# Kernel tuning notes

Hardware: AMD Instinct MI355X
Metric: run time of the kernel (lower is better)

## Reference

```python
import jax, jax.numpy as jnp
import numpy as np

N_NODES = 100000
N_EDGES = 600000
N_GRAPHS = 64
BN_EPS = 1e-5


def setup_inputs() -> dict:
    key = jax.random.key(0)
    ks = jax.random.split(key, 32)
    inp = {
        "x": jax.random.normal(ks[0], (N_NODES, 128), dtype=jnp.float32),
        "edge_index": jax.random.randint(ks[1], (2, N_EDGES), 0, N_NODES, dtype=jnp.int64),
        "batch": jnp.sort(jax.random.randint(ks[2], (N_NODES,), 0, N_GRAPHS, dtype=jnp.int64)),
    }
    dims = [(128, 64, 64), (64, 64, 64), (64, 64, 96)]  # (in, hid, out) per GIN layer
    ki = 3
    for i, (d_in, d_hid, d_out) in enumerate(dims):
        inp[f"l{i}_w1"] = jax.random.normal(ks[ki], (d_in, d_hid), dtype=jnp.float32) * 0.05; ki += 1
        inp[f"l{i}_b1"] = jnp.zeros((d_hid,), dtype=jnp.float32)
        inp[f"l{i}_w2"] = jax.random.normal(ks[ki], (d_hid, d_out), dtype=jnp.float32) * 0.05; ki += 1
        inp[f"l{i}_b2"] = jnp.zeros((d_out,), dtype=jnp.float32)
        inp[f"bn{i}_g"] = jax.random.uniform(ks[ki], (d_out,), minval=0.5, maxval=1.5, dtype=jnp.float32); ki += 1
        inp[f"bn{i}_b"] = jax.random.normal(ks[ki], (d_out,), dtype=jnp.float32) * 0.05; ki += 1
        inp[f"bn{i}_m"] = jax.random.normal(ks[ki], (d_out,), dtype=jnp.float32) * 0.05; ki += 1
        inp[f"bn{i}_v"] = jax.random.uniform(ks[ki], (d_out,), minval=0.5, maxval=1.5, dtype=jnp.float32); ki += 1
    return inp


def _gin_layer(x, src, dst, w1, b1, w2, b2, g, bb, m, v):
    # GINConv (eps=0): h_i = MLP(x_i + sum_{j: j->i} x_j)
    aggr = jax.ops.segment_sum(x[src], dst, num_segments=N_NODES)
    h = x + aggr
    h = jax.nn.relu(h @ w1 + b1) @ w2 + b2
    # eval-mode BatchNorm1d + ReLU
    h = (h - m) * jax.lax.rsqrt(v + BN_EPS) * g + bb
    return jax.nn.relu(h)


def reference(x, edge_index, batch,
              l0_w1, l0_b1, l0_w2, l0_b2, bn0_g, bn0_b, bn0_m, bn0_v,
              l1_w1, l1_b1, l1_w2, l1_b2, bn1_g, bn1_b, bn1_m, bn1_v,
              l2_w1, l2_b1, l2_w2, l2_b2, bn2_g, bn2_b, bn2_m, bn2_v):
    src, dst = edge_index[0], edge_index[1]
    h = _gin_layer(x, src, dst, l0_w1, l0_b1, l0_w2, l0_b2, bn0_g, bn0_b, bn0_m, bn0_v)
    h = _gin_layer(h, src, dst, l1_w1, l1_b1, l1_w2, l1_b2, bn1_g, bn1_b, bn1_m, bn1_v)
    h = _gin_layer(h, src, dst, l2_w1, l2_b1, l2_w2, l2_b2, bn2_g, bn2_b, bn2_m, bn2_v)
    # global mean pool over graphs
    sums = jax.ops.segment_sum(h, batch, num_segments=N_GRAPHS)
    counts = jax.ops.segment_sum(jnp.ones((h.shape[0],), dtype=h.dtype), batch, num_segments=N_GRAPHS)
    return sums / jnp.maximum(counts, 1.0)[:, None]
```

## Files before the change

### kernel.cpp

```cpp
#include <hip/hip_runtime.h>

#define N_NODES 100000
#define N_GRAPHS 64
#define N_EDGES 600000
#define BN_EPS 1e-5f

__global__ void deg_hist_kernel(const int* __restrict__ dst,
                                int* __restrict__ deg, int n_edges) {
    int e = blockIdx.x * blockDim.x + threadIdx.x;
    if (e < n_edges) atomicAdd(&deg[dst[e]], 1);
}

__global__ void scan1_kernel(const int* __restrict__ deg, int* __restrict__ excl,
                             int* __restrict__ partials, int n) {
    __shared__ int s[1024];
    int i = blockIdx.x * 1024 + threadIdx.x;
    int v = (i < n) ? deg[i] : 0;
    s[threadIdx.x] = v;
    __syncthreads();
    for (int off = 1; off < 1024; off <<= 1) {
        int t = (threadIdx.x >= (unsigned)off) ? s[threadIdx.x - off] : 0;
        __syncthreads();
        s[threadIdx.x] += t;
        __syncthreads();
    }
    if (i < n) excl[i] = s[threadIdx.x] - v;
    if (threadIdx.x == 1023) partials[blockIdx.x] = s[1023];
}

__global__ void scan2_kernel(int* partials, int nb) {
    __shared__ int s[128];
    int t = threadIdx.x;
    int v = (t < nb) ? partials[t] : 0;
    s[t] = v;
    __syncthreads();
    for (int off = 1; off < 128; off <<= 1) {
        int u = (t >= off) ? s[t - off] : 0;
        __syncthreads();
        s[t] += u;
        __syncthreads();
    }
    if (t < nb) partials[t] = s[t] - v;
}

__global__ void scan3_kernel(int* __restrict__ rowptr, const int* __restrict__ partials,
                             int n, int total) {
    int i = blockIdx.x * blockDim.x + threadIdx.x;
    if (i < n) rowptr[i] += partials[i >> 10];
    else if (i == n) rowptr[n] = total;
}

__global__ void csr_fill_kernel(const int* __restrict__ src, const int* __restrict__ dst,
                                const int* __restrict__ rowptr, int* __restrict__ cursor,
                                int* __restrict__ eids, int n_edges) {
    int e = blockIdx.x * blockDim.x + threadIdx.x;
    if (e >= n_edges) return;
    int t = dst[e];
    int pos = rowptr[t] + atomicAdd(&cursor[t], 1);
    eids[pos] = src[e];
}

__global__ void graph_bounds_kernel(const int* __restrict__ batch,
                                    int* __restrict__ gstart, int n_nodes) {
    int n = blockIdx.x * blockDim.x + threadIdx.x;
    if (n >= n_nodes) return;
    if (n == 0) {
        for (int g = 0; g <= batch[0]; ++g) gstart[g] = 0;
    } else {
        int b0 = batch[n - 1], b1 = batch[n];
        for (int g = b0 + 1; g <= b1; ++g) gstart[g] = n;
    }
    if (n == n_nodes - 1) {
        for (int g = batch[n] + 1; g <= N_GRAPHS; ++g) gstart[g] = n_nodes;
    }
}

__global__ void prep_kernel(const float* __restrict__ w1, const float* __restrict__ w2,
                            const float* __restrict__ b2, const float* __restrict__ g,
                            const float* __restrict__ bb, const float* __restrict__ m,
                            const float* __restrict__ v,
                            float* __restrict__ w1T, float* __restrict__ w2sT,
                            float* __restrict__ bias2, int DIN, int DOUT) {
    int i = blockIdx.x * blockDim.x + threadIdx.x;
    if (i < 64 * DIN) {
        int j = i / DIN, k = i % DIN;
        w1T[i] = w1[k * 64 + j];
    }
    int i2 = i - 64 * DIN;
    if (i2 >= 0 && i2 < DOUT * 64) {
        int c = i2 / 64, j = i2 % 64;
        float s = g[c] * rsqrtf(v[c] + BN_EPS);
        w2sT[i2] = w2[j * DOUT + c] * s;
    }
    int i3 = i2 - DOUT * 64;
    if (i3 >= 0 && i3 < DOUT) {
        float s = g[i3] * rsqrtf(v[i3] + BN_EPS);
        bias2[i3] = (b2[i3] - m[i3]) * s + bb[i3];
    }
}

__global__ __launch_bounds__(256)
void pre_gemm_kernel(const float* __restrict__ x, const float* __restrict__ w1T,
                     float* __restrict__ y, int n_nodes) {
    __shared__ float w1s[64 * 128];
    const int tid = threadIdx.x;
    const long base = (long)blockIdx.x * 64;

    const float4* gw1 = (const float4*)w1T;
    for (int i4 = tid; i4 < 16 * 128; i4 += 256) {
        int row = i4 >> 5, k4 = i4 & 31;
        *(float4*)&w1s[row * 128 + ((k4 ^ ((row >> 2) & 7)) << 2)] = gw1[i4];
    }
    __syncthreads();

    const int jg = tid & 15, ng = tid >> 4, xw = jg & 7;
    const float* wp = &w1s[(jg * 4) * 128];
    const float4* xv = (const float4*)x;
    long r[4];
    #pragma unroll
    for (int i = 0; i < 4; ++i) {
        long rr = base + ng * 4 + i;
        r[i] = (rr < n_nodes) ? rr : (n_nodes - 1);
    }
    float acc[4][4] = {};
    #pragma unroll 4
    for (int k4 = 0; k4 < 32; ++k4) {
        const int ko = (k4 ^ xw) << 2;
        float4 w0 = *(const float4*)&wp[0 * 128 + ko];
        float4 w1v = *(const float4*)&wp[1 * 128 + ko];
        float4 w2v = *(const float4*)&wp[2 * 128 + ko];
        float4 w3v = *(const float4*)&wp[3 * 128 + ko];
        #pragma unroll
        for (int i = 0; i < 4; ++i) {
            float4 a = xv[r[i] * 32 + k4];
            acc[i][0] = fmaf(a.x, w0.x, fmaf(a.y, w0.y, fmaf(a.z, w0.z, fmaf(a.w, w0.w, acc[i][0]))));
            acc[i][1] = fmaf(a.x, w1v.x, fmaf(a.y, w1v.y, fmaf(a.z, w1v.z, fmaf(a.w, w1v.w, acc[i][1]))));
            acc[i][2] = fmaf(a.x, w2v.x, fmaf(a.y, w2v.y, fmaf(a.z, w2v.z, fmaf(a.w, w2v.w, acc[i][2]))));
            acc[i][3] = fmaf(a.x, w3v.x, fmaf(a.y, w3v.y, fmaf(a.z, w3v.z, fmaf(a.w, w3v.w, acc[i][3]))));
        }
    }
    #pragma unroll
    for (int i = 0; i < 4; ++i) {
        long n = base + ng * 4 + i;
        if (n < n_nodes) {
            float4 v = {acc[i][0], acc[i][1], acc[i][2], acc[i][3]};
            *(float4*)(y + n * 64 + jg * 4) = v;
        }
    }
}

__global__ __launch_bounds__(256)
void gather64_kernel(const float* __restrict__ y, const int* __restrict__ rowptr,
                     const int* __restrict__ eids, const float* __restrict__ b1,
                     float* __restrict__ t, int n_nodes) {
    int node = blockIdx.x * 16 + (threadIdx.x >> 4);
    if (node >= n_nodes) return;
    int f4 = threadIdx.x & 15;
    const float4* yv = (const float4*)y;
    float4 acc = yv[(long)node * 16 + f4];
    int b = rowptr[node], e = rowptr[node + 1];
    int i = b;
    for (; i + 3 < e; i += 4) {
        int s0 = eids[i], s1 = eids[i + 1], s2 = eids[i + 2], s3 = eids[i + 3];
        float4 r0 = yv[(long)s0 * 16 + f4];
        float4 r1 = yv[(long)s1 * 16 + f4];
        float4 r2 = yv[(long)s2 * 16 + f4];
        float4 r3 = yv[(long)s3 * 16 + f4];
        acc.x += (r0.x + r1.x) + (r2.x + r3.x);
        acc.y += (r0.y + r1.y) + (r2.y + r3.y);
        acc.z += (r0.z + r1.z) + (r2.z + r3.z);
        acc.w += (r0.w + r1.w) + (r2.w + r3.w);
    }
    for (; i < e; ++i) {
        int s = eids[i];
        float4 r = yv[(long)s * 16 + f4];
        acc.x += r.x; acc.y += r.y; acc.z += r.z; acc.w += r.w;
    }
    float4 bv = ((const float4*)b1)[f4];
    float4 o;
    o.x = fmaxf(acc.x + bv.x, 0.0f);
    o.y = fmaxf(acc.y + bv.y, 0.0f);
    o.z = fmaxf(acc.z + bv.z, 0.0f);
    o.w = fmaxf(acc.w + bv.w, 0.0f);
    ((float4*)t)[(long)node * 16 + f4] = o;
}

__global__ __launch_bounds__(256)
void fused_mid_kernel(const float* __restrict__ t, const float* __restrict__ w2sT,
                      const float* __restrict__ bias2, const float* __restrict__ w1nT,
                      float* __restrict__ ynext, int n_nodes) {
    constexpr int SS = 68;
    __shared__ float sT[64 * SS];
    __shared__ float wbuf[64 * 64];
    const int tid = threadIdx.x;
    const long base = (long)blockIdx.x * 64;

    const float4* gw2 = (const float4*)w2sT;
    for (int i4 = tid; i4 < 16 * 64; i4 += 256) {
        int row = i4 >> 4, k4 = i4 & 15;
        *(float4*)&wbuf[row * 64 + ((k4 ^ ((row >> 2) & 7)) << 2)] = gw2[i4];
    }
    __syncthreads();

    const int jg = tid & 15, ng = tid >> 4, xw = jg & 7;
    const float4* tv = (const float4*)(t + base * 64);

    float h[4][4];
    {
        const float* wp = &wbuf[(jg * 4) * 64];
        float acc[4][4] = {};
        #pragma unroll 4
        for (int k4 = 0; k4 < 16; ++k4) {
            const int ko = (k4 ^ xw) << 2;
            float4 w0 = *(const float4*)&wp[0 * 64 + ko];
            float4 w1v = *(const float4*)&wp[1 * 64 + ko];
            float4 w2v = *(const float4*)&wp[2 * 64 + ko];
            float4 w3v = *(const float4*)&wp[3 * 64 + ko];
            #pragma unroll
            for (int i = 0; i < 4; ++i) {
                float4 a = tv[(ng * 4 + i) * 16 + k4];
                acc[i][0] = fmaf(a.x, w0.x, fmaf(a.y, w0.y, fmaf(a.z, w0.z, fmaf(a.w, w0.w, acc[i][0]))));
                acc[i][1] = fmaf(a.x, w1v.x, fmaf(a.y, w1v.y, fmaf(a.z, w1v.z, fmaf(a.w, w1v.w, acc[i][1]))));
                acc[i][2] = fmaf(a.x, w2v.x, fmaf(a.y, w2v.y, fmaf(a.z, w2v.z, fmaf(a.w, w2v.w, acc[i][2]))));
                acc[i][3] = fmaf(a.x, w3v.x, fmaf(a.y, w3v.y, fmaf(a.z, w3v.z, fmaf(a.w, w3v.w, acc[i][3]))));
            }
        }
        float4 bv = *(const float4*)&bias2[jg * 4];
        #pragma unroll
        for (int i = 0; i < 4; ++i) {
            h[i][0] = fmaxf(acc[i][0] + bv.x, 0.0f);
            h[i][1] = fmaxf(acc[i][1] + bv.y, 0.0f);
            h[i][2] = fmaxf(acc[i][2] + bv.z, 0.0f);
            h[i][3] = fmaxf(acc[i][3] + bv.w, 0.0f);
        }
    }
    __syncthreads();

    #pragma unroll
    for (int i = 0; i < 4; ++i) {
        float4 hv = {h[i][0], h[i][1], h[i][2], h[i][3]};
        *(float4*)&sT[(ng * 4 + i) * SS + jg * 4] = hv;
    }
    const float4* gw1n = (const float4*)w1nT;
    for (int i4 = tid; i4 < 16 * 64; i4 += 256) {
        int row = i4 >> 4, k4 = i4 & 15;
        *(float4*)&wbuf[row * 64 + ((k4 ^ ((row >> 2) & 7)) << 2)] = gw1n[i4];
    }
    __syncthreads();

    {
        const float* ap = &sT[(ng * 4) * SS];
        const float* wp = &wbuf[(jg * 4) * 64];
        float acc[4][4] = {};
        #pragma unroll 4
        for (int k4 = 0; k4 < 16; ++k4) {
            const int ko = (k4 ^ xw) << 2;
            float4 w0 = *(const float4*)&wp[0 * 64 + ko];
            float4 w1v = *(const float4*)&wp[1 * 64 + ko];
            float4 w2v = *(const float4*)&wp[2 * 64 + ko];
            float4 w3v = *(const float4*)&wp[3 * 64 + ko];
            #pragma unroll
            for (int i = 0; i < 4; ++i) {
                float4 a = *(const float4*)&ap[i * SS + k4 * 4];
                acc[i][0] = fmaf(a.x, w0.x, fmaf(a.y, w0.y, fmaf(a.z, w0.z, fmaf(a.w, w0.w, acc[i][0]))));
                acc[i][1] = fmaf(a.x, w1v.x, fmaf(a.y, w1v.y, fmaf(a.z, w1v.z, fmaf(a.w, w1v.w, acc[i][1]))));
                acc[i][2] = fmaf(a.x, w2v.x, fmaf(a.y, w2v.y, fmaf(a.z, w2v.z, fmaf(a.w, w2v.w, acc[i][2]))));
                acc[i][3] = fmaf(a.x, w3v.x, fmaf(a.y, w3v.y, fmaf(a.z, w3v.z, fmaf(a.w, w3v.w, acc[i][3]))));
            }
        }
        #pragma unroll
        for (int i = 0; i < 4; ++i) {
            long n = base + ng * 4 + i;
            if (n < n_nodes) {
                float4 v = {acc[i][0], acc[i][1], acc[i][2], acc[i][3]};
                *(float4*)(ynext + n * 64 + jg * 4) = v;
            }
        }
    }
}

__global__ __launch_bounds__(256)
void fused_final_kernel(const float* __restrict__ t, const float* __restrict__ w2sT,
                        const float* __restrict__ bias2, float* __restrict__ out,
                        int n_nodes) {
    constexpr int CPT = 6;
    __shared__ float w2s[96 * 64];
    const int tid = threadIdx.x;
    const long base = (long)blockIdx.x * 64;

    const float4* gw2 = (const float4*)w2sT;
    for (int i4 = tid; i4 < 96 * 16; i4 += 256) {
        int row = i4 >> 4, k4 = i4 & 15;
        *(float4*)&w2s[row * 64 + ((k4 ^ ((row / CPT) & 7)) << 2)] = gw2[i4];
    }
    __syncthreads();

    const int cg = tid & 15, ng = tid >> 4, xw = cg & 7;
    const float4* tv = (const float4*)(t + base * 64);
    const float* wp = &w2s[(cg * CPT) * 64];
    float acc[4][CPT] = {};
    #pragma unroll 4
    for (int k4 = 0; k4 < 16; ++k4) {
        const int ko = (k4 ^ xw) << 2;
        float4 wv[CPT];
        #pragma unroll
        for (int c = 0; c < CPT; ++c) wv[c] = *(const float4*)&wp[c * 64 + ko];
        #pragma unroll
        for (int i = 0; i < 4; ++i) {
            float4 h = tv[(ng * 4 + i) * 16 + k4];
            #pragma unroll
            for (int c = 0; c < CPT; ++c)
                acc[i][c] = fmaf(h.x, wv[c].x, fmaf(h.y, wv[c].y, fmaf(h.z, wv[c].z, fmaf(h.w, wv[c].w, acc[i][c]))));
        }
    }
    float bv[CPT];
    #pragma unroll
    for (int c = 0; c < CPT; ++c) bv[c] = bias2[cg * CPT + c];
    #pragma unroll
    for (int i = 0; i < 4; ++i) {
        long n = base + ng * 4 + i;
        if (n < n_nodes) {
            float* op = out + n * 96 + cg * CPT;
            #pragma unroll
            for (int c = 0; c < CPT; ++c) op[c] = fmaxf(acc[i][c] + bv[c], 0.0f);
        }
    }
}

#define POOL_SPLIT 16
__global__ __launch_bounds__(192)
void pool_seg_kernel(const float* __restrict__ h, const int* __restrict__ gstart,
                     float* __restrict__ sums) {
    int g = blockIdx.x >> 4;
    int s = blockIdx.x & 15;
    int lo = gstart[g], hi = gstart[g + 1];
    int len = hi - lo;
    int seg = (len + POOL_SPLIT - 1) / POOL_SPLIT;
    int a = lo + s * seg;
    int b = a + seg; if (b > hi) b = hi;

    int f4 = threadIdx.x % 24;
    int chain = threadIdx.x / 24;
    const float4* hv = (const float4*)h;
    float4 acc = {0.0f, 0.0f, 0.0f, 0.0f};
    for (int n = a + chain; n < b; n += 8) {
        float4 v = hv[(long)n * 24 + f4];
        acc.x += v.x; acc.y += v.y; acc.z += v.z; acc.w += v.w;
    }
    __shared__ float4 red[8][24];
    red[chain][f4] = acc;
    __syncthreads();
    if (threadIdx.x < 24) {
        float4 t = red[0][threadIdx.x];
        #pragma unroll
        for (int c = 1; c < 8; ++c) {
            float4 r = red[c][threadIdx.x];
            t.x += r.x; t.y += r.y; t.z += r.z; t.w += r.w;
        }
        float* sp = &sums[g * 96 + threadIdx.x * 4];
        atomicAdd(sp + 0, t.x);
        atomicAdd(sp + 1, t.y);
        atomicAdd(sp + 2, t.z);
        atomicAdd(sp + 3, t.w);
    }
}

__global__ void finalize_kernel(const float* __restrict__ sums,
                                const int* __restrict__ gstart,
                                float* __restrict__ out) {
    int i = blockIdx.x * blockDim.x + threadIdx.x;
    if (i >= N_GRAPHS * 96) return;
    int g = i / 96;
    float cnt = (float)(gstart[g + 1] - gstart[g]);
    out[i] = sums[i] / fmaxf(cnt, 1.0f);
}

static inline int cdiv_l(long a, int b) { return (int)((a + b - 1) / b); }

extern "C" void kernel_launch(void* const* d_in, const int* in_sizes, int n_in,
                              void* d_out, int out_size, void* d_ws, size_t ws_size,
                              hipStream_t stream) {
    const float* x     = (const float*)d_in[0];
    const int*   ei    = (const int*)d_in[1];
    const int*   src   = ei;
    const int*   dst   = ei + N_EDGES;
    const int*   batch = (const int*)d_in[2];

    const float* P[3][8];
    int p = 3;
    for (int l = 0; l < 3; ++l)
        for (int q = 0; q < 8; ++q)
            P[l][q] = (const float*)d_in[p++];

    const long NP = N_NODES + 64;
    float* ws   = (float*)d_ws;
    float* yT   = ws;
    float* gB   = yT + NP * 64;
    float* h2   = gB + NP * 64;
    float* q    = h2 + NP * 96;
    float* w1T[3], *w2sT[3], *bias2[3];
    for (int l = 0; l < 3; ++l) {
        w1T[l] = q;   q += 64 * 128;
        w2sT[l] = q;  q += 96 * 64;
        bias2[l] = q; q += 96;
    }
    float* sums   = q;
    int* gstart   = (int*)(sums + N_GRAPHS * 96);
    int* deg      = gstart + 72;
    int* cursor   = deg + N_NODES;
    int* partials = cursor + N_NODES;
    int* rowptr   = partials + 128;
    int* eids     = rowptr + (N_NODES + 1);

    const int B = 256;
    const int DIN[3]  = {128, 64, 64};
    const int DOUT[3] = {64, 64, 96};

    for (int l = 0; l < 3; ++l) {
        int tot = 64 * DIN[l] + 64 * DOUT[l] + DOUT[l];
        prep_kernel<<<cdiv_l(tot, B), B, 0, stream>>>(
            P[l][0], P[l][2], P[l][3], P[l][4], P[l][5], P[l][6], P[l][7],
            w1T[l], w2sT[l], bias2[l], DIN[l], DOUT[l]);
    }

    hipMemsetAsync(deg, 0, (size_t)(2 * N_NODES + 128) * sizeof(int), stream);
    deg_hist_kernel<<<cdiv_l(N_EDGES, B), B, 0, stream>>>(dst, deg, N_EDGES);
    int nblk = cdiv_l(N_NODES, 1024);
    scan1_kernel<<<nblk, 1024, 0, stream>>>(deg, rowptr, partials, N_NODES);
    scan2_kernel<<<1, 128, 0, stream>>>(partials, nblk);
    scan3_kernel<<<cdiv_l(N_NODES + 1, B), B, 0, stream>>>(rowptr, partials, N_NODES, N_EDGES);
    csr_fill_kernel<<<cdiv_l(N_EDGES, B), B, 0, stream>>>(src, dst, rowptr, cursor, eids, N_EDGES);
    graph_bounds_kernel<<<cdiv_l(N_NODES, B), B, 0, stream>>>(batch, gstart, N_NODES);

    const int ntiles = cdiv_l(N_NODES, 64);
    const int ngather = cdiv_l(N_NODES, 16);

    pre_gemm_kernel<<<ntiles, 256, 0, stream>>>(x, w1T[0], yT, N_NODES);
    gather64_kernel<<<ngather, 256, 0, stream>>>(yT, rowptr, eids, P[0][1], gB, N_NODES);
    fused_mid_kernel<<<ntiles, 256, 0, stream>>>(
        gB, w2sT[0], bias2[0], w1T[1], yT, N_NODES);
    gather64_kernel<<<ngather, 256, 0, stream>>>(yT, rowptr, eids, P[1][1], gB, N_NODES);
    fused_mid_kernel<<<ntiles, 256, 0, stream>>>(
        gB, w2sT[1], bias2[1], w1T[2], yT, N_NODES);
    gather64_kernel<<<ngather, 256, 0, stream>>>(yT, rowptr, eids, P[2][1], gB, N_NODES);
    fused_final_kernel<<<ntiles, 256, 0, stream>>>(
        gB, w2sT[2], bias2[2], h2, N_NODES);

    hipMemsetAsync(sums, 0, (size_t)(N_GRAPHS * 96) * sizeof(float), stream);
    pool_seg_kernel<<<N_GRAPHS * POOL_SPLIT, 192, 0, stream>>>(h2, gstart, sums);
    finalize_kernel<<<cdiv_l(N_GRAPHS * 96, B), B, 0, stream>>>(
        sums, gstart, (float*)d_out);
}
```

Baseline: 433.4 us.

## Fuse neighbor gather into MLP kernels with 128-node tiles and ping-pong buffers

Each per-layer gather kernel is folded into the following MLP kernel: the block gathers neighbor rows for its 128-node tile straight into shared memory and then runs both GEMMs, so the intermediate buffer no longer makes a global round trip. Tiles and blocks grow to 128 nodes and 512 threads, the three prep launches become one 2D launch, and pooling writes per-split partials that finalize sums, replacing the atomics and memset. In exchange, the latency-bound gather now shares a block with heavy shared-memory use (about 51 KB), which may lower occupancy and leave fewer warps to hide gather latency.

```diff
diff --git a/kernel.cpp b/kernel.cpp
--- a/kernel.cpp
+++ b/kernel.cpp
@@ -75,39 +75,42 @@
     }
 }
 
-__global__ void prep_kernel(const float* __restrict__ w1, const float* __restrict__ w2,
-                            const float* __restrict__ b2, const float* __restrict__ g,
-                            const float* __restrict__ bb, const float* __restrict__ m,
-                            const float* __restrict__ v,
-                            float* __restrict__ w1T, float* __restrict__ w2sT,
-                            float* __restrict__ bias2, int DIN, int DOUT) {
+struct LayerPrep {
+    const float *w1, *w2, *b2, *g, *bb, *m, *v;
+    float *w1T, *w2sT, *bias2;
+    int DIN, DOUT;
+};
+struct PrepAll { LayerPrep l[3]; };
+
+__global__ void prep_all_kernel(PrepAll pa) {
+    LayerPrep P = pa.l[blockIdx.y];
     int i = blockIdx.x * blockDim.x + threadIdx.x;
-    if (i < 64 * DIN) {
-        int j = i / DIN, k = i % DIN;
-        w1T[i] = w1[k * 64 + j];
-    }
-    int i2 = i - 64 * DIN;
-    if (i2 >= 0 && i2 < DOUT * 64) {
+    if (i < 64 * P.DIN) {
+        int j = i / P.DIN, k = i % P.DIN;
+        P.w1T[i] = P.w1[k * 64 + j];
+    }
+    int i2 = i - 64 * P.DIN;
+    if (i2 >= 0 && i2 < P.DOUT * 64) {
         int c = i2 / 64, j = i2 % 64;
-        float s = g[c] * rsqrtf(v[c] + BN_EPS);
-        w2sT[i2] = w2[j * DOUT + c] * s;
-    }
-    int i3 = i2 - DOUT * 64;
-    if (i3 >= 0 && i3 < DOUT) {
-        float s = g[i3] * rsqrtf(v[i3] + BN_EPS);
-        bias2[i3] = (b2[i3] - m[i3]) * s + bb[i3];
-    }
-}
-
-__global__ __launch_bounds__(256)
+        float s = P.g[c] * rsqrtf(P.v[c] + BN_EPS);
+        P.w2sT[i2] = P.w2[j * P.DOUT + c] * s;
+    }
+    int i3 = i2 - P.DOUT * 64;
+    if (i3 >= 0 && i3 < P.DOUT) {
+        float s = P.g[i3] * rsqrtf(P.v[i3] + BN_EPS);
+        P.bias2[i3] = (P.b2[i3] - P.m[i3]) * s + P.bb[i3];
+    }
+}
+
+__global__ __launch_bounds__(512)
 void pre_gemm_kernel(const float* __restrict__ x, const float* __restrict__ w1T,
                      float* __restrict__ y, int n_nodes) {
     __shared__ float w1s[64 * 128];
     const int tid = threadIdx.x;
-    const long base = (long)blockIdx.x * 64;
+    const long base = (long)blockIdx.x * 128;
 
     const float4* gw1 = (const float4*)w1T;
-    for (int i4 = tid; i4 < 16 * 128; i4 += 256) {
+    for (int i4 = tid; i4 < 16 * 128; i4 += 512) {
         int row = i4 >> 5, k4 = i4 & 31;
         *(float4*)&w1s[row * 128 + ((k4 ^ ((row >> 2) & 7)) << 2)] = gw1[i4];
     }
@@ -149,105 +152,74 @@
     }
 }
 
-__global__ __launch_bounds__(256)
-void gather64_kernel(const float* __restrict__ y, const int* __restrict__ rowptr,
-                     const int* __restrict__ eids, const float* __restrict__ b1,
-                     float* __restrict__ t, int n_nodes) {
-    int node = blockIdx.x * 16 + (threadIdx.x >> 4);
-    if (node >= n_nodes) return;
-    int f4 = threadIdx.x & 15;
+template <int SS>
+__device__ __forceinline__ void gather_tile(const float* __restrict__ y,
+                                            const int* __restrict__ rowptr,
+                                            const int* __restrict__ eids,
+                                            const float* __restrict__ b1,
+                                            float* sT, long base, int n_nodes,
+                                            int tid) {
     const float4* yv = (const float4*)y;
-    float4 acc = yv[(long)node * 16 + f4];
-    int b = rowptr[node], e = rowptr[node + 1];
-    int i = b;
-    for (; i + 3 < e; i += 4) {
-        int s0 = eids[i], s1 = eids[i + 1], s2 = eids[i + 2], s3 = eids[i + 3];
-        float4 r0 = yv[(long)s0 * 16 + f4];
-        float4 r1 = yv[(long)s1 * 16 + f4];
-        float4 r2 = yv[(long)s2 * 16 + f4];
-        float4 r3 = yv[(long)s3 * 16 + f4];
-        acc.x += (r0.x + r1.x) + (r2.x + r3.x);
-        acc.y += (r0.y + r1.y) + (r2.y + r3.y);
-        acc.z += (r0.z + r1.z) + (r2.z + r3.z);
-        acc.w += (r0.w + r1.w) + (r2.w + r3.w);
-    }
-    for (; i < e; ++i) {
-        int s = eids[i];
-        float4 r = yv[(long)s * 16 + f4];
-        acc.x += r.x; acc.y += r.y; acc.z += r.z; acc.w += r.w;
-    }
-    float4 bv = ((const float4*)b1)[f4];
-    float4 o;
-    o.x = fmaxf(acc.x + bv.x, 0.0f);
-    o.y = fmaxf(acc.y + bv.y, 0.0f);
-    o.z = fmaxf(acc.z + bv.z, 0.0f);
-    o.w = fmaxf(acc.w + bv.w, 0.0f);
-    ((float4*)t)[(long)node * 16 + f4] = o;
-}
-
-__global__ __launch_bounds__(256)
-void fused_mid_kernel(const float* __restrict__ t, const float* __restrict__ w2sT,
-                      const float* __restrict__ bias2, const float* __restrict__ w1nT,
-                      float* __restrict__ ynext, int n_nodes) {
+    const int f4 = tid & 15;
+    const float4 bv = ((const float4*)b1)[f4];
+    #pragma unroll
+    for (int pass = 0; pass < 4; ++pass) {
+        int nl = pass * 32 + (tid >> 4);
+        long node = base + nl;
+        float4 acc = {0.0f, 0.0f, 0.0f, 0.0f};
+        if (node < n_nodes) {
+            acc = yv[node * 16 + f4];
+            int b = rowptr[node], e = rowptr[node + 1];
+            int i = b;
+            for (; i + 3 < e; i += 4) {
+                int s0 = eids[i], s1 = eids[i + 1], s2 = eids[i + 2], s3 = eids[i + 3];
+                float4 r0 = yv[(long)s0 * 16 + f4];
+                float4 r1 = yv[(long)s1 * 16 + f4];
+                float4 r2 = yv[(long)s2 * 16 + f4];
+                float4 r3 = yv[(long)s3 * 16 + f4];
+                acc.x += (r0.x + r1.x) + (r2.x + r3.x);
+                acc.y += (r0.y + r1.y) + (r2.y + r3.y);
+                acc.z += (r0.z + r1.z) + (r2.z + r3.z);
+                acc.w += (r0.w + r1.w) + (r2.w + r3.w);
+            }
+            for (; i < e; ++i) {
+                int s = eids[i];
+                float4 r = yv[(long)s * 16 + f4];
+                acc.x += r.x; acc.y += r.y; acc.z += r.z; acc.w += r.w;
+            }
+        }
+        float4 o;
+        o.x = fmaxf(acc.x + bv.x, 0.0f);
+        o.y = fmaxf(acc.y + bv.y, 0.0f);
+        o.z = fmaxf(acc.z + bv.z, 0.0f);
+        o.w = fmaxf(acc.w + bv.w, 0.0f);
+        *(float4*)&sT[nl * SS + f4 * 4] = o;
+    }
+}
+
+__global__ __launch_bounds__(512)
+void mlp_mid_kernel(const float* __restrict__ y, const int* __restrict__ rowptr,
+                    const int* __restrict__ eids, const float* __restrict__ b1,
+                    const float* __restrict__ w2sT, const float* __restrict__ bias2,
+                    const float* __restrict__ w1nT, float* __restrict__ ynext,
+                    int n_nodes) {
     constexpr int SS = 68;
-    __shared__ float sT[64 * SS];
+    __shared__ float sT[128 * SS];
     __shared__ float wbuf[64 * 64];
     const int tid = threadIdx.x;
-    const long base = (long)blockIdx.x * 64;
+    const long base = (long)blockIdx.x * 128;
 
     const float4* gw2 = (const float4*)w2sT;
-    for (int i4 = tid; i4 < 16 * 64; i4 += 256) {
+    for (int i4 = tid; i4 < 16 * 64; i4 += 512) {
         int row = i4 >> 4, k4 = i4 & 15;
         *(float4*)&wbuf[row * 64 + ((k4 ^ ((row >> 2) & 7)) << 2)] = gw2[i4];
     }
+    gather_tile<SS>(y, rowptr, eids, b1, sT, base, n_nodes, tid);
     __syncthreads();
 
     const int jg = tid & 15, ng = tid >> 4, xw = jg & 7;
-    const float4* tv = (const float4*)(t + base * 64);
 
     float h[4][4];
-    {
-        const float* wp = &wbuf[(jg * 4) * 64];
-        float acc[4][4] = {};
-        #pragma unroll 4
-        for (int k4 = 0; k4 < 16; ++k4) {
-            const int ko = (k4 ^ xw) << 2;
-            float4 w0 = *(const float4*)&wp[0 * 64 + ko];
-            float4 w1v = *(const float4*)&wp[1 * 64 + ko];
-            float4 w2v = *(const float4*)&wp[2 * 64 + ko];
-            float4 w3v = *(const float4*)&wp[3 * 64 + ko];
-            #pragma unroll
-            for (int i = 0; i < 4; ++i) {
-                float4 a = tv[(ng * 4 + i) * 16 + k4];
-                acc[i][0] = fmaf(a.x, w0.x, fmaf(a.y, w0.y, fmaf(a.z, w0.z, fmaf(a.w, w0.w, acc[i][0]))));
-                acc[i][1] = fmaf(a.x, w1v.x, fmaf(a.y, w1v.y, fmaf(a.z, w1v.z, fmaf(a.w, w1v.w, acc[i][1]))));
-                acc[i][2] = fmaf(a.x, w2v.x, fmaf(a.y, w2v.y, fmaf(a.z, w2v.z, fmaf(a.w, w2v.w, acc[i][2]))));
-                acc[i][3] = fmaf(a.x, w3v.x, fmaf(a.y, w3v.y, fmaf(a.z, w3v.z, fmaf(a.w, w3v.w, acc[i][3]))));
-            }
-        }
-        float4 bv = *(const float4*)&bias2[jg * 4];
-        #pragma unroll
-        for (int i = 0; i < 4; ++i) {
-            h[i][0] = fmaxf(acc[i][0] + bv.x, 0.0f);
-            h[i][1] = fmaxf(acc[i][1] + bv.y, 0.0f);
-            h[i][2] = fmaxf(acc[i][2] + bv.z, 0.0f);
-            h[i][3] = fmaxf(acc[i][3] + bv.w, 0.0f);
-        }
-    }
-    __syncthreads();
-
-    #pragma unroll
-    for (int i = 0; i < 4; ++i) {
-        float4 hv = {h[i][0], h[i][1], h[i][2], h[i][3]};
-        *(float4*)&sT[(ng * 4 + i) * SS + jg * 4] = hv;
-    }
-    const float4* gw1n = (const float4*)w1nT;
-    for (int i4 = tid; i4 < 16 * 64; i4 += 256) {
-        int row = i4 >> 4, k4 = i4 & 15;
-        *(float4*)&wbuf[row * 64 + ((k4 ^ ((row >> 2) & 7)) << 2)] = gw1n[i4];
-    }
-    __syncthreads();
-
     {
         const float* ap = &sT[(ng * 4) * SS];
         const float* wp = &wbuf[(jg * 4) * 64];
@@ -268,6 +240,49 @@
                 acc[i][3] = fmaf(a.x, w3v.x, fmaf(a.y, w3v.y, fmaf(a.z, w3v.z, fmaf(a.w, w3v.w, acc[i][3]))));
             }
         }
+        float4 bv = *(const float4*)&bias2[jg * 4];
+        #pragma unroll
+        for (int i = 0; i < 4; ++i) {
+            h[i][0] = fmaxf(acc[i][0] + bv.x, 0.0f);
+            h[i][1] = fmaxf(acc[i][1] + bv.y, 0.0f);
+            h[i][2] = fmaxf(acc[i][2] + bv.z, 0.0f);
+            h[i][3] = fmaxf(acc[i][3] + bv.w, 0.0f);
+        }
+    }
+    __syncthreads();
+
+    #pragma unroll
+    for (int i = 0; i < 4; ++i) {
+        float4 hv = {h[i][0], h[i][1], h[i][2], h[i][3]};
+        *(float4*)&sT[(ng * 4 + i) * SS + jg * 4] = hv;
+    }
+    const float4* gw1n = (const float4*)w1nT;
+    for (int i4 = tid; i4 < 16 * 64; i4 += 512) {
+        int row = i4 >> 4, k4 = i4 & 15;
+        *(float4*)&wbuf[row * 64 + ((k4 ^ ((row >> 2) & 7)) << 2)] = gw1n[i4];
+    }
+    __syncthreads();
+
+    {
+        const float* ap = &sT[(ng * 4) * SS];
+        const float* wp = &wbuf[(jg * 4) * 64];
+        float acc[4][4] = {};
+        #pragma unroll 4
+        for (int k4 = 0; k4 < 16; ++k4) {
+            const int ko = (k4 ^ xw) << 2;
+            float4 w0 = *(const float4*)&wp[0 * 64 + ko];
+            float4 w1v = *(const float4*)&wp[1 * 64 + ko];
+            float4 w2v = *(const float4*)&wp[2 * 64 + ko];
+            float4 w3v = *(const float4*)&wp[3 * 64 + ko];
+            #pragma unroll
+            for (int i = 0; i < 4; ++i) {
+                float4 a = *(const float4*)&ap[i * SS + k4 * 4];
+                acc[i][0] = fmaf(a.x, w0.x, fmaf(a.y, w0.y, fmaf(a.z, w0.z, fmaf(a.w, w0.w, acc[i][0]))));
+                acc[i][1] = fmaf(a.x, w1v.x, fmaf(a.y, w1v.y, fmaf(a.z, w1v.z, fmaf(a.w, w1v.w, acc[i][1]))));
+                acc[i][2] = fmaf(a.x, w2v.x, fmaf(a.y, w2v.y, fmaf(a.z, w2v.z, fmaf(a.w, w2v.w, acc[i][2]))));
+                acc[i][3] = fmaf(a.x, w3v.x, fmaf(a.y, w3v.y, fmaf(a.z, w3v.z, fmaf(a.w, w3v.w, acc[i][3]))));
+            }
+        }
         #pragma unroll
         for (int i = 0; i < 4; ++i) {
             long n = base + ng * 4 + i;
@@ -279,24 +294,28 @@
     }
 }
 
-__global__ __launch_bounds__(256)
-void fused_final_kernel(const float* __restrict__ t, const float* __restrict__ w2sT,
-                        const float* __restrict__ bias2, float* __restrict__ out,
-                        int n_nodes) {
+__global__ __launch_bounds__(512)
+void mlp_final_kernel(const float* __restrict__ y, const int* __restrict__ rowptr,
+                      const int* __restrict__ eids, const float* __restrict__ b1,
+                      const float* __restrict__ w2sT, const float* __restrict__ bias2,
+                      float* __restrict__ out, int n_nodes) {
+    constexpr int SS = 68;
     constexpr int CPT = 6;
+    __shared__ float sT[128 * SS];
     __shared__ float w2s[96 * 64];
     const int tid = threadIdx.x;
-    const long base = (long)blockIdx.x * 64;
+    const long base = (long)blockIdx.x * 128;
 
     const float4* gw2 = (const float4*)w2sT;
-    for (int i4 = tid; i4 < 96 * 16; i4 += 256) {
+    for (int i4 = tid; i4 < 96 * 16; i4 += 512) {
         int row = i4 >> 4, k4 = i4 & 15;
         *(float4*)&w2s[row * 64 + ((k4 ^ ((row / CPT) & 7)) << 2)] = gw2[i4];
     }
+    gather_tile<SS>(y, rowptr, eids, b1, sT, base, n_nodes, tid);
     __syncthreads();
 
     const int cg = tid & 15, ng = tid >> 4, xw = cg & 7;
-    const float4* tv = (const float4*)(t + base * 64);
+    const float* hp = &sT[(ng * 4) * SS];
     const float* wp = &w2s[(cg * CPT) * 64];
     float acc[4][CPT] = {};
     #pragma unroll 4
@@ -307,7 +326,7 @@
         for (int c = 0; c < CPT; ++c) wv[c] = *(const float4*)&wp[c * 64 + ko];
         #pragma unroll
         for (int i = 0; i < 4; ++i) {
-            float4 h = tv[(ng * 4 + i) * 16 + k4];
+            float4 h = *(const float4*)&hp[i * SS + k4 * 4];
             #pragma unroll
             for (int c = 0; c < CPT; ++c)
                 acc[i][c] = fmaf(h.x, wv[c].x, fmaf(h.y, wv[c].y, fmaf(h.z, wv[c].z, fmaf(h.w, wv[c].w, acc[i][c]))));
@@ -330,7 +349,7 @@
 #define POOL_SPLIT 16
 __global__ __launch_bounds__(192)
 void pool_seg_kernel(const float* __restrict__ h, const int* __restrict__ gstart,
-                     float* __restrict__ sums) {
+                     float* __restrict__ part) {
     int g = blockIdx.x >> 4;
     int s = blockIdx.x & 15;
     int lo = gstart[g], hi = gstart[g + 1];
@@ -357,22 +376,21 @@
             float4 r = red[c][threadIdx.x];
             t.x += r.x; t.y += r.y; t.z += r.z; t.w += r.w;
         }
-        float* sp = &sums[g * 96 + threadIdx.x * 4];
-        atomicAdd(sp + 0, t.x);
-        atomicAdd(sp + 1, t.y);
-        atomicAdd(sp + 2, t.z);
-        atomicAdd(sp + 3, t.w);
-    }
-}
-
-__global__ void finalize_kernel(const float* __restrict__ sums,
+        *(float4*)&part[((long)blockIdx.x) * 96 + threadIdx.x * 4] = t;
+    }
+}
+
+__global__ void finalize_kernel(const float* __restrict__ part,
                                 const int* __restrict__ gstart,
                                 float* __restrict__ out) {
     int i = blockIdx.x * blockDim.x + threadIdx.x;
     if (i >= N_GRAPHS * 96) return;
-    int g = i / 96;
+    int g = i / 96, c = i - g * 96;
+    float s = 0.0f;
+    #pragma unroll
+    for (int k = 0; k < POOL_SPLIT; ++k) s += part[((long)g * POOL_SPLIT + k) * 96 + c];
     float cnt = (float)(gstart[g + 1] - gstart[g]);
-    out[i] = sums[i] / fmaxf(cnt, 1.0f);
+    out[i] = s / fmaxf(cnt, 1.0f);
 }
 
 static inline int cdiv_l(long a, int b) { return (int)((a + b - 1) / b); }
@@ -392,11 +410,11 @@
         for (int q = 0; q < 8; ++q)
             P[l][q] = (const float*)d_in[p++];
 
-    const long NP = N_NODES + 64;
+    const long NP = N_NODES + 128;
     float* ws   = (float*)d_ws;
-    float* yT   = ws;
-    float* gB   = yT + NP * 64;
-    float* h2   = gB + NP * 64;
+    float* yA   = ws;
+    float* yB   = yA + NP * 64;
+    float* h2   = yB + NP * 64;
     float* q    = h2 + NP * 96;
     float* w1T[3], *w2sT[3], *bias2[3];
     for (int l = 0; l < 3; ++l) {
@@ -404,8 +422,8 @@
         w2sT[l] = q;  q += 96 * 64;
         bias2[l] = q; q += 96;
     }
-    float* sums   = q;
-    int* gstart   = (int*)(sums + N_GRAPHS * 96);
+    float* part   = q;
+    int* gstart   = (int*)(part + N_GRAPHS * POOL_SPLIT * 96);
     int* deg      = gstart + 72;
     int* cursor   = deg + N_NODES;
     int* partials = cursor + N_NODES;
@@ -416,12 +434,16 @@
     const int DIN[3]  = {128, 64, 64};
     const int DOUT[3] = {64, 64, 96};
 
+    PrepAll pa;
     for (int l = 0; l < 3; ++l) {
-        int tot = 64 * DIN[l] + 64 * DOUT[l] + DOUT[l];
-        prep_kernel<<<cdiv_l(tot, B), B, 0, stream>>>(
-            P[l][0], P[l][2], P[l][3], P[l][4], P[l][5], P[l][6], P[l][7],
-            w1T[l], w2sT[l], bias2[l], DIN[l], DOUT[l]);
-    }
+        pa.l[l].w1 = P[l][0]; pa.l[l].w2 = P[l][2]; pa.l[l].b2 = P[l][3];
+        pa.l[l].g = P[l][4];  pa.l[l].bb = P[l][5]; pa.l[l].m = P[l][6];
+        pa.l[l].v = P[l][7];
+        pa.l[l].w1T = w1T[l]; pa.l[l].w2sT = w2sT[l]; pa.l[l].bias2 = bias2[l];
+        pa.l[l].DIN = DIN[l]; pa.l[l].DOUT = DOUT[l];
+    }
+    dim3 pgrid(cdiv_l(64 * 128 + 96 * 64 + 96, B), 3);
+    prep_all_kernel<<<pgrid, B, 0, stream>>>(pa);
 
     hipMemsetAsync(deg, 0, (size_t)(2 * N_NODES + 128) * sizeof(int), stream);
     deg_hist_kernel<<<cdiv_l(N_EDGES, B), B, 0, stream>>>(dst, deg, N_EDGES);
@@ -432,22 +454,17 @@
     csr_fill_kernel<<<cdiv_l(N_EDGES, B), B, 0, stream>>>(src, dst, rowptr, cursor, eids, N_EDGES);
     graph_bounds_kernel<<<cdiv_l(N_NODES, B), B, 0, stream>>>(batch, gstart, N_NODES);
 
-    const int ntiles = cdiv_l(N_NODES, 64);
-    const int ngather = cdiv_l(N_NODES, 16);
-
-    pre_gemm_kernel<<<ntiles, 256, 0, stream>>>(x, w1T[0], yT, N_NODES);
-    gather64_kernel<<<ngather, 256, 0, stream>>>(yT, rowptr, eids, P[0][1], gB, N_NODES);
-    fused_mid_kernel<<<ntiles, 256, 0, stream>>>(
-        gB, w2sT[0], bias2[0], w1T[1], yT, N_NODES);
-    gather64_kernel<<<ngather, 256, 0, stream>>>(yT, rowptr, eids, P[1][1], gB, N_NODES);
-    fused_mid_kernel<<<ntiles, 256, 0, stream>>>(
-        gB, w2sT[1], bias2[1], w1T[2], yT, N_NODES);
-    gather64_kernel<<<ngather, 256, 0, stream>>>(yT, rowptr, eids, P[2][1], gB, N_NODES);
-    fused_final_kernel<<<ntiles, 256, 0, stream>>>(
-        gB, w2sT[2], bias2[2], h2, N_NODES);
-
-    hipMemsetAsync(sums, 0, (size_t)(N_GRAPHS * 96) * sizeof(float), stream);
-    pool_seg_kernel<<<N_GRAPHS * POOL_SPLIT, 192, 0, stream>>>(h2, gstart, sums);
+    const int ntiles = cdiv_l(N_NODES, 128);
+
+    pre_gemm_kernel<<<ntiles, 512, 0, stream>>>(x, w1T[0], yA, N_NODES);
+    mlp_mid_kernel<<<ntiles, 512, 0, stream>>>(
+        yA, rowptr, eids, P[0][1], w2sT[0], bias2[0], w1T[1], yB, N_NODES);
+    mlp_mid_kernel<<<ntiles, 512, 0, stream>>>(
+        yB, rowptr, eids, P[1][1], w2sT[1], bias2[1], w1T[2], yA, N_NODES);
+    mlp_final_kernel<<<ntiles, 512, 0, stream>>>(
+        yA, rowptr, eids, P[2][1], w2sT[2], bias2[2], h2, N_NODES);
+
+    pool_seg_kernel<<<N_GRAPHS * POOL_SPLIT, 192, 0, stream>>>(h2, gstart, part);
     finalize_kernel<<<cdiv_l(N_GRAPHS * 96, B), B, 0, stream>>>(
-        sums, gstart, (float*)d_out);
-}
+        part, gstart, (float*)d_out);
+}
```

New measurement: 462.7 us. 1.07x slower.
